# Performance work log

Hardware: AMD Instinct MI355X
Metric: run time of the kernel (lower is better)

Reference implementation:

```python
import jax, jax.numpy as jnp
import numpy as np

DIM = 1024
NUM_HEADS = 16
HEAD_DIM = 64

def setup_inputs() -> dict:
    key = jax.random.key(0)
    ks = jax.random.split(key, 7)
    x = jax.random.normal(ks[0], (4, 4096, DIM), dtype=jnp.float32)
    mask = jnp.ones((4, 4096), dtype=jnp.float32)
    # torch Linear stores weight (out, in) and computes x @ W.T; we store (in, out) directly.
    Wq = jax.random.normal(ks[1], (DIM, NUM_HEADS * HEAD_DIM), dtype=jnp.float32) / np.sqrt(DIM)
    Wk = jax.random.normal(ks[2], (DIM, NUM_HEADS * HEAD_DIM), dtype=jnp.float32) / np.sqrt(DIM)
    Wv = jax.random.normal(ks[3], (DIM, NUM_HEADS * HEAD_DIM), dtype=jnp.float32) / np.sqrt(DIM)
    Wo = jax.random.normal(ks[4], (NUM_HEADS * HEAD_DIM, DIM), dtype=jnp.float32) / np.sqrt(NUM_HEADS * HEAD_DIM)
    # FeatureMap buffer: randn(dim, dim) / sqrt(dim) with dim = head_dim
    proj = jax.random.normal(ks[5], (HEAD_DIM, HEAD_DIM), dtype=jnp.float32) / np.sqrt(HEAD_DIM)
    return {"x": x, "mask": mask, "Wq": Wq, "Wk": Wk, "Wv": Wv, "Wo": Wo, "proj": proj}

def _feature_map(x, proj):
    # phi(x) = elu(x @ proj) + 1  (non-negative random features)
    return jax.nn.elu(x @ proj) + 1.0

def reference(x, mask, Wq, Wk, Wv, Wo, proj):
    b, n, _ = x.shape
    h, d = NUM_HEADS, HEAD_DIM
    # project and split heads: (b, h, n, d)
    q = (x @ Wq).reshape(b, n, h, d).transpose(0, 2, 1, 3)
    k = (x @ Wk).reshape(b, n, h, d).transpose(0, 2, 1, 3)
    v = (x @ Wv).reshape(b, n, h, d).transpose(0, 2, 1, 3)
    q = _feature_map(q, proj)
    k = _feature_map(k, proj)
    # mask: (b, n) -> (b, 1, n, 1)
    k = k * mask[:, None, :, None]
    # linear attention: phi(Q) (phi(K)^T V)
    kv = jnp.einsum('bhnd,bhne->bhde', k, v)          # (b, h, d, d)
    qkv = jnp.einsum('bhnd,bhde->bhne', q, kv)        # (b, h, n, d)
    k_sum = k.sum(axis=2)                              # (b, h, d)
    normalizer = jnp.einsum('bhnd,bhd->bhn', q, k_sum) + 1e-06
    out = qkv / normalizer[..., None]
    out = out.transpose(0, 2, 1, 3).reshape(b, n, h * d)
    return out @ Wo
```

## Files before the change

### kernel.cpp

```cpp
#include <hip/hip_runtime.h>
#include <stdint.h>

#define TOKENS 16384
#define KDIM 1024
#define QKVN 3072

typedef unsigned short u16;
using bf16x8 = __attribute__((ext_vector_type(8))) __bf16;
using f32x4  = __attribute__((ext_vector_type(4))) float;
using u16x8  = __attribute__((ext_vector_type(8))) unsigned short;

__device__ inline u16 f2bf(float f) {
  union { float f; uint32_t u; } v; v.f = f;
  uint32_t u = v.u;
  return (u16)((u + 0x7FFFu + ((u >> 16) & 1u)) >> 16);
}
__device__ inline float bf2f(u16 s) {
  union { uint32_t u; float f; } v; v.u = ((uint32_t)s) << 16;
  return v.f;
}
__device__ inline void g2l16(const void* g, void* l) {
  __builtin_amdgcn_global_load_lds(
      (const __attribute__((address_space(1))) void*)g,
      (__attribute__((address_space(3))) void*)l, 16, 0, 0);
}

template<int LD>
__device__ inline void stage_half(const u16* __restrict__ g, u16* l, int t) {
  #pragma unroll
  for (int i = 0; i < 2; ++i) {
    const int ch = i * 512 + t;
    const int row = ch >> 3;
    const int cc = (ch & 7) ^ (row & 7);
    g2l16(g + (long)row * LD + cc * 8, (char*)l + ch * 16);
  }
}

#define LDA_H(DST, BASE) do { \
  _Pragma("unroll") \
  for (int mi = 0; mi < 4; ++mi) { \
    const int row = wm*64 + mi*16 + rl; \
    const char* p = (const char*)(BASE) + row*128; \
    const int sw = (row & 7) << 4; \
    DST[mi][0] = *(const bf16x8*)(p + ((kg*16) ^ sw)); \
    DST[mi][1] = *(const bf16x8*)(p + ((64 + kg*16) ^ sw)); \
  } \
} while (0)

#define LDB_H(DST, BASE) do { \
  _Pragma("unroll") \
  for (int ni = 0; ni < 2; ++ni) { \
    const int row = wn*32 + ni*16 + rl; \
    const char* p = (const char*)(BASE) + row*128; \
    const int sw = (row & 7) << 4; \
    DST[ni][0] = *(const bf16x8*)(p + ((kg*16) ^ sw)); \
    DST[ni][1] = *(const bf16x8*)(p + ((64 + kg*16) ^ sw)); \
  } \
} while (0)

#define MFMA2Q(MH, AV, BV0, BV1) do { \
  __builtin_amdgcn_s_setprio(1); \
  _Pragma("unroll") \
  for (int kh = 0; kh < 2; ++kh) \
    _Pragma("unroll") \
    for (int mi = 0; mi < 4; ++mi) \
      _Pragma("unroll") \
      for (int ni = 0; ni < 2; ++ni) { \
        acc[(MH)*4+mi][ni]   = __builtin_amdgcn_mfma_f32_16x16x32_bf16( \
            AV[mi][kh], BV0[ni][kh], acc[(MH)*4+mi][ni], 0, 0, 0); \
        acc[(MH)*4+mi][2+ni] = __builtin_amdgcn_mfma_f32_16x16x32_bf16( \
            AV[mi][kh], BV1[ni][kh], acc[(MH)*4+mi][2+ni], 0, 0, 0); \
      } \
  __builtin_amdgcn_s_setprio(0); \
} while (0)

#define LGKM0 do { \
  asm volatile("s_waitcnt lgkmcnt(0)" ::: "memory"); \
  __builtin_amdgcn_sched_barrier(0); \
} while (0)
#define VMC(N) asm volatile("s_waitcnt vmcnt(" #N ")" ::: "memory")
#define BAR() __builtin_amdgcn_s_barrier()

template<int NTOT, int EPI, int ALD, int NT, int PERB>
__device__ __forceinline__ void gemm_body(
    const u16* __restrict__ A, const u16* __restrict__ Bm,
    void* __restrict__ C, const float* __restrict__ aux) {
  __shared__ u16 As[2][2][8192];
  __shared__ u16 Bs[2][2][8192];
  const int t = threadIdx.x;
  const int l = t & 63;
  const int w = t >> 6;
  const int rl = l & 15, kg = l >> 4;
  const int wm = w >> 2, wn = w & 3;
  constexpr int nbn = NTOT / 256;
  constexpr int nwg = 64 * nbn;
  constexpr int GRID = nwg / NT;
  constexpr int KC = NT * 16;
  constexpr int IT = KC / 2;
  static_assert(nwg % 8 == 0, "bijective xcd swizzle");
  const int bid = blockIdx.x;

  auto tcoord = [&](int ot, long& tar, long& tbr) {
    const int gt = ot * GRID + bid;
    const int swz = (gt & 7) * (nwg / 8) + (gt >> 3);
    tar = (long)(swz / nbn) * 256;
    tbr = (long)(swz % nbn) * 256;
  };
  auto asrc = [&](int ch) {
    long ta, tb; tcoord(ch >> 4, ta, tb);
    return A + ta * ALD + (ch & 15) * 64;
  };
  auto bsrc = [&](int ch) {
    long ta, tb; tcoord(ch >> 4, ta, tb);
    return Bm + (PERB ? (ta >> 12) * 1048576 : 0) + tb * 1024 + (ch & 15) * 64;
  };

  f32x4 acc[8][4];
  #pragma unroll
  for (int i = 0; i < 8; ++i)
    #pragma unroll
    for (int j = 0; j < 4; ++j)
      acc[i][j] = (f32x4){0.f, 0.f, 0.f, 0.f};

  bf16x8 afA[4][2], bA[2][2], bB[2][2];

  auto epilogue = [&](int ot) {
    long ar0, br0; tcoord(ot, ar0, br0);
    #pragma unroll
    for (int mh = 0; mh < 2; ++mh)
      #pragma unroll
      for (int mi = 0; mi < 4; ++mi)
        #pragma unroll
        for (int j = 0; j < 4; ++j) {
          const long row = ar0 + mh*128 + wm*64 + mi*16 + kg*4 + j;
          float rs = 0.f;
          if (EPI == 0) rs = aux[row];
          #pragma unroll
          for (int nh = 0; nh < 2; ++nh)
            #pragma unroll
            for (int ni = 0; ni < 2; ++ni) {
              const long col = br0 + nh*128 + wn*32 + ni*16 + rl;
              float v = acc[mh*4+mi][nh*2+ni][j];
              if (EPI == 0) {
                if (col < 2048) {
                  v = (v > 0.f) ? (v + 1.f) : __expf(v);
                  if (col >= 1024) v *= rs;
                }
                ((u16*)C)[row * QKVN + col] = f2bf(v);
              } else {
                ((float*)C)[row * NTOT + col] = v;
              }
            }
        }
    #pragma unroll
    for (int i = 0; i < 8; ++i)
      #pragma unroll
      for (int j = 0; j < 4; ++j)
        acc[i][j] = (f32x4){0.f, 0.f, 0.f, 0.f};
  };

  {
    const u16* A0s = asrc(0); const u16* B0s = bsrc(0);
    const u16* A1s = asrc(1); const u16* B1s = bsrc(1);
    stage_half<ALD >(A0s,             As[0][0], t);
    stage_half<1024>(B0s,             Bs[0][0], t);
    stage_half<1024>(B0s + 128*1024,  Bs[0][1], t);
    stage_half<ALD >(A0s + 128*ALD,   As[0][1], t);
    stage_half<ALD >(A1s,             As[1][0], t);
    stage_half<1024>(B1s,             Bs[1][0], t);
    VMC(4);
    BAR();
  }

  for (int i = 0; i < IT; ++i) {
    const int o1 = 2*i + 1;
    const int e = (2*i + 2 < KC) ? 2*i + 2 : KC - 1;
    const int o = (2*i + 3 < KC) ? 2*i + 3 : KC - 1;
    const u16* Ao1 = asrc(o1); const u16* Bo1 = bsrc(o1);
    const u16* Ae = asrc(e);   const u16* Be = bsrc(e);
    const u16* Ao = asrc(o);   const u16* Bo = bsrc(o);

    LDA_H(afA, As[0][0]); LDB_H(bA, Bs[0][0]); LDB_H(bB, Bs[0][1]);
    stage_half<ALD>(Ao1 + 128*ALD, As[1][1], t);
    stage_half<1024>(Bo1 + 128*1024, Bs[1][1], t);
    LGKM0;
    MFMA2Q(0, afA, bA, bB);
    BAR();

    LDA_H(afA, As[0][1]);
    stage_half<ALD>(Ae, As[0][0], t);
    stage_half<1024>(Be, Bs[0][0], t);
    LGKM0;
    MFMA2Q(1, afA, bA, bB);
    VMC(4); BAR();

    LDA_H(afA, As[1][0]); LDB_H(bA, Bs[1][0]); LDB_H(bB, Bs[1][1]);
    stage_half<ALD>(Ae + 128*ALD, As[0][1], t);
    stage_half<1024>(Be + 128*1024, Bs[0][1], t);
    LGKM0;
    MFMA2Q(0, afA, bA, bB);
    BAR();

    LDA_H(afA, As[1][1]);
    stage_half<ALD>(Ao, As[1][0], t);
    stage_half<1024>(Bo, Bs[1][0], t);
    LGKM0;
    MFMA2Q(1, afA, bA, bB);
    VMC(4); BAR();

    if ((i & 7) == 7) epilogue(i >> 3);
  }
  VMC(0);
}

__global__ __launch_bounds__(512, 2) void gemm_qkv(
    const u16* __restrict__ A, const u16* __restrict__ Bm,
    void* __restrict__ C, const float* __restrict__ aux) {
  gemm_body<3072, 0, 1024, 3, 0>(A, Bm, C, aux);
}
__global__ __launch_bounds__(512, 2) void gemm_out(
    const u16* __restrict__ A, const u16* __restrict__ Bm,
    void* __restrict__ C, const float* __restrict__ aux) {
  gemm_body<1024, 1, 1024, 1, 1>(A, Bm, C, aux);
}

__global__ __launch_bounds__(256) void kv_kernel(const u16* __restrict__ QKV,
    float* __restrict__ kvws, float* __restrict__ ksws) {
  __shared__ u16 Kl[32 * 64];
  __shared__ u16 Vl[32 * 64];
  const int t = threadIdx.x;
  const int l = t & 63, w = t >> 6;
  const int rl = l & 15, kg = l >> 4;
  const int bid = blockIdx.x;
  const int bh = bid >> 4, ns = bid & 15;
  const int b = bh >> 4, h = bh & 15;
  const long tok0 = (long)b * 4096 + ns * 256;

  f32x4 acc[4];
  #pragma unroll
  for (int i = 0; i < 4; ++i) acc[i] = (f32x4){0.f, 0.f, 0.f, 0.f};
  float ks = 0.f;
  const int srow = t >> 3, scc = t & 7;

  for (int it = 0; it < 8; ++it) {
    const long tb = tok0 + it * 32;
    g2l16(QKV + (tb + srow) * QKVN + 1024 + h * 64 + scc * 8, (char*)Kl + t * 16);
    g2l16(QKV + (tb + srow) * QKVN + 2048 + h * 64 + scc * 8, (char*)Vl + t * 16);
    __syncthreads();
    union { u16x8 u; bf16x8 v; } au, bu;
    #pragma unroll
    for (int j = 0; j < 8; ++j) au.u[j] = Kl[(kg * 8 + j) * 64 + w * 16 + rl];
    #pragma unroll
    for (int ni = 0; ni < 4; ++ni) {
      #pragma unroll
      for (int j = 0; j < 8; ++j) bu.u[j] = Vl[(kg * 8 + j) * 64 + ni * 16 + rl];
      acc[ni] = __builtin_amdgcn_mfma_f32_16x16x32_bf16(au.v, bu.v, acc[ni], 0, 0, 0);
    }
    #pragma unroll
    for (int r = 0; r < 8; ++r) ks += bf2f(Kl[(w * 8 + r) * 64 + (t & 63)]);
    __syncthreads();
  }
  float* kvb = kvws + bh * 4096;
  #pragma unroll
  for (int ni = 0; ni < 4; ++ni)
    #pragma unroll
    for (int j = 0; j < 4; ++j) {
      const int d = w * 16 + kg * 4 + j;
      const int e = ni * 16 + rl;
      atomicAdd(&kvb[d * 64 + e], acc[ni][j]);
    }
  atomicAdd(&ksws[bh * 64 + (t & 63)], ks);
}

__global__ __launch_bounds__(256) void finish_kernel(const u16* __restrict__ QKV,
    const float* __restrict__ ksws, const float* __restrict__ kvws,
    const float* __restrict__ Wo, u16* __restrict__ Qc, u16* __restrict__ W2T) {
  __shared__ float sh[4096];
  const int t = threadIdx.x;
  if (blockIdx.x < 1024) {
    const int bid = blockIdx.x;
    const int n0 = bid * 16;
    const int b = n0 >> 12;
    #pragma unroll
    for (int i = 0; i < 4; ++i) sh[i * 256 + t] = ksws[b * 1024 + i * 256 + t];
    __syncthreads();
    const int h = t & 15, ti = t >> 4;
    const u16* qp = QKV + (long)(n0 + ti) * QKVN + h * 64;
    u16* op = Qc + (long)(n0 + ti) * 1024 + h * 64;
    u16x8 v[8];
    float norm = 1e-6f;
    #pragma unroll
    for (int i = 0; i < 8; ++i) {
      v[i] = *(const u16x8*)(qp + i * 8);
      #pragma unroll
      for (int j = 0; j < 8; ++j) norm += bf2f(v[i][j]) * sh[h * 64 + i * 8 + j];
    }
    const float inv = 1.0f / norm;
    #pragma unroll
    for (int i = 0; i < 8; ++i) {
      u16x8 o;
      #pragma unroll
      for (int j = 0; j < 8; ++j) o[j] = f2bf(bf2f(v[i][j]) * inv);
      *(u16x8*)(op + i * 8) = o;
    }
  } else {
    const int bid = blockIdx.x - 1024;
    const int bh = bid >> 2, os = bid & 3;
    const int b = bh >> 4, h = bh & 15;
    const float* kvb = kvws + bh * 4096;
    #pragma unroll
    for (int i = 0; i < 16; ++i) sh[i * 256 + t] = kvb[i * 256 + t];
    __syncthreads();
    const int o = os * 256 + t;
    float wo[64];
    #pragma unroll
    for (int e = 0; e < 64; ++e) wo[e] = Wo[(long)(h * 64 + e) * 1024 + o];
    u16* out = W2T + (long)b * 1048576 + (long)o * 1024 + h * 64;
    for (int d = 0; d < 64; ++d) {
      float s = 0.f;
      #pragma unroll
      for (int e = 0; e < 64; ++e) s += wo[e] * sh[d * 64 + e];
      out[d] = f2bf(s);
    }
  }
}

__global__ __launch_bounds__(256) void prep_w(const float* __restrict__ Wq,
    const float* __restrict__ Wk, const float* __restrict__ proj,
    const float* __restrict__ Wv, const float* __restrict__ x,
    u16* __restrict__ WqkvT, u16* __restrict__ xb) {
  __shared__ float Wl[128][65];
  __shared__ float Pl[64][65];
  const int t = threadIdx.x;
  if (blockIdx.x >= 512) {
    const int idx = (blockIdx.x - 512) * 256 + t;
    const float4* p = (const float4*)x + (long)idx * 2;
    const float4 a = p[0], b = p[1];
    u16x8 o;
    o[0] = f2bf(a.x); o[1] = f2bf(a.y); o[2] = f2bf(a.z); o[3] = f2bf(a.w);
    o[4] = f2bf(b.x); o[5] = f2bf(b.y); o[6] = f2bf(b.z); o[7] = f2bf(b.w);
    *((u16x8*)xb + idx) = o;
    return;
  }
  if (blockIdx.x < 256) {
    const int bid = blockIdx.x;
    const int m = bid >> 7, h = (bid >> 3) & 15, cb = bid & 7;
    const float* W = m ? Wk : Wq;
    #pragma unroll
    for (int i = 0; i < 16; ++i) {
      const int idx = i * 256 + t;
      Pl[idx >> 6][idx & 63] = proj[idx];
    }
    #pragma unroll
    for (int i = 0; i < 32; ++i) {
      const int idx = i * 256 + t;
      const int c = idx >> 6, d = idx & 63;
      Wl[c][d] = W[(long)(cb * 128 + c) * 1024 + h * 64 + d];
    }
    __syncthreads();
    const int c = t & 127, j0 = (t >> 7) * 32;
    float a[32];
    #pragma unroll
    for (int jj = 0; jj < 32; ++jj) a[jj] = 0.f;
    for (int d = 0; d < 64; ++d) {
      const float wv = Wl[c][d];
      #pragma unroll
      for (int jj = 0; jj < 32; ++jj) a[jj] += wv * Pl[d][j0 + jj];
    }
    #pragma unroll
    for (int jj = 0; jj < 32; ++jj)
      WqkvT[(long)(m * 1024 + h * 64 + j0 + jj) * 1024 + cb * 128 + c] = f2bf(a[jj]);
  } else {
    const int bid = blockIdx.x - 256;
    const int rt = (bid >> 4) & 15, ct = bid & 15;
    const int j = t & 63;
    #pragma unroll
    for (int p = 0; p < 16; ++p) {
      const int i = p * 4 + (t >> 6);
      Wl[i][j] = Wv[(long)(rt * 64 + i) * 1024 + ct * 64 + j];
    }
    __syncthreads();
    u16* dst = WqkvT + (long)2048 * 1024;
    #pragma unroll
    for (int p = 0; p < 16; ++p) {
      const int i = p * 4 + (t >> 6);
      dst[(long)(ct * 64 + i) * 1024 + rt * 64 + j] = f2bf(Wl[j][i]);
    }
  }
}

extern "C" void kernel_launch(void* const* d_in, const int* in_sizes, int n_in,
                              void* d_out, int out_size, void* d_ws, size_t ws_size,
                              hipStream_t stream) {
  const float* x    = (const float*)d_in[0];
  const float* mask = (const float*)d_in[1];
  const float* Wq   = (const float*)d_in[2];
  const float* Wk   = (const float*)d_in[3];
  const float* Wv   = (const float*)d_in[4];
  const float* Wo   = (const float*)d_in[5];
  const float* proj = (const float*)d_in[6];

  char* ws = (char*)d_ws;
  u16*  WqkvT = (u16*)(ws);
  u16*  xb    = (u16*)(ws + 8388608);
  u16*  QKV   = (u16*)(ws + 41943040);
  float* kvws = (float*)(ws + 142606336);
  float* ksws = (float*)(ws + 143654912);
  u16*  Qc   = xb;
  u16*  W2T  = (u16*)(ws);
  if (ws_size < (size_t)143671296) return;

  hipMemsetAsync(kvws, 0, 1064960, stream);
  prep_w<<<8704, 256, 0, stream>>>(Wq, Wk, proj, Wv, x, WqkvT, xb);
  gemm_qkv<<<256, 512, 0, stream>>>(xb, WqkvT, (void*)QKV, mask);
  kv_kernel<<<1024, 256, 0, stream>>>(QKV, kvws, ksws);
  finish_kernel<<<1280, 256, 0, stream>>>(QKV, ksws, kvws, Wo, Qc, W2T);
  gemm_out<<<256, 512, 0, stream>>>(Qc, W2T, d_out, nullptr);
}
```

Before: 235.2 us.

## Software-pipeline LDS fragment loads with double register buffers in GEMM mainloop

Adds a second A-fragment register buffer so the next half-tile's LDS reads are issued before the current MFMA block, and waits on partial lgkmcnt instead of draining to zero. B-fragment loads for the next chunk move to after the MFMAs, and global-to-LDS staging of B halves is regrouped with adjusted vmcnt thresholds. The aim is to hide LDS read latency behind MFMA work in both the QKV and output GEMMs. In exchange it raises register pressure under launch_bounds(512,2), and the hand-set wait counts must exactly match the number of outstanding loads or the kernel reads stale data.

```diff
diff --git a/kernel.cpp b/kernel.cpp
--- a/kernel.cpp
+++ b/kernel.cpp
@@ -74,8 +74,8 @@
   __builtin_amdgcn_s_setprio(0); \
 } while (0)
 
-#define LGKM0 do { \
-  asm volatile("s_waitcnt lgkmcnt(0)" ::: "memory"); \
+#define LGKMW(N) do { \
+  asm volatile("s_waitcnt lgkmcnt(" #N ")" ::: "memory"); \
   __builtin_amdgcn_sched_barrier(0); \
 } while (0)
 #define VMC(N) asm volatile("s_waitcnt vmcnt(" #N ")" ::: "memory")
@@ -122,7 +122,7 @@
     for (int j = 0; j < 4; ++j)
       acc[i][j] = (f32x4){0.f, 0.f, 0.f, 0.f};
 
-  bf16x8 afA[4][2], bA[2][2], bB[2][2];
+  bf16x8 afA[4][2], afB[4][2], bA[2][2], bB[2][2];
 
   auto epilogue = [&](int ot) {
     long ar0, br0; tcoord(ot, ar0, br0);
@@ -168,49 +168,62 @@
     stage_half<ALD >(A0s + 128*ALD,   As[0][1], t);
     stage_half<ALD >(A1s,             As[1][0], t);
     stage_half<1024>(B1s,             Bs[1][0], t);
-    VMC(4);
+    stage_half<1024>(B1s + 128*1024,  Bs[1][1], t);
+    VMC(8);
     BAR();
+    LDA_H(afA, As[0][0]);
+    LDB_H(bA, Bs[0][0]);
+    LDB_H(bB, Bs[0][1]);
   }
 
   for (int i = 0; i < IT; ++i) {
     const int o1 = 2*i + 1;
     const int e = (2*i + 2 < KC) ? 2*i + 2 : KC - 1;
     const int o = (2*i + 3 < KC) ? 2*i + 3 : KC - 1;
-    const u16* Ao1 = asrc(o1); const u16* Bo1 = bsrc(o1);
+    const u16* Ao1 = asrc(o1);
     const u16* Ae = asrc(e);   const u16* Be = bsrc(e);
     const u16* Ao = asrc(o);   const u16* Bo = bsrc(o);
 
-    LDA_H(afA, As[0][0]); LDB_H(bA, Bs[0][0]); LDB_H(bB, Bs[0][1]);
+    VMC(6);
+    LDA_H(afB, As[0][1]);
     stage_half<ALD>(Ao1 + 128*ALD, As[1][1], t);
-    stage_half<1024>(Bo1 + 128*1024, Bs[1][1], t);
-    LGKM0;
+    LGKMW(8);
     MFMA2Q(0, afA, bA, bB);
     BAR();
 
-    LDA_H(afA, As[0][1]);
-    stage_half<ALD>(Ae, As[0][0], t);
-    stage_half<1024>(Be, Bs[0][0], t);
-    LGKM0;
-    MFMA2Q(1, afA, bA, bB);
-    VMC(4); BAR();
-
-    LDA_H(afA, As[1][0]); LDB_H(bA, Bs[1][0]); LDB_H(bB, Bs[1][1]);
+    VMC(2);
+    LDA_H(afA, As[1][0]);
+    stage_half<ALD >(Ae,             As[0][0], t);
+    stage_half<1024>(Be,             Bs[0][0], t);
+    stage_half<1024>(Be + 128*1024,  Bs[0][1], t);
+    LGKMW(8);
+    MFMA2Q(1, afB, bA, bB);
+    LDB_H(bA, Bs[1][0]);
+    LDB_H(bB, Bs[1][1]);
+    BAR();
+
+    VMC(6);
+    LDA_H(afB, As[1][1]);
     stage_half<ALD>(Ae + 128*ALD, As[0][1], t);
-    stage_half<1024>(Be + 128*1024, Bs[0][1], t);
-    LGKM0;
+    LGKMW(8);
     MFMA2Q(0, afA, bA, bB);
     BAR();
 
-    LDA_H(afA, As[1][1]);
-    stage_half<ALD>(Ao, As[1][0], t);
-    stage_half<1024>(Bo, Bs[1][0], t);
-    LGKM0;
-    MFMA2Q(1, afA, bA, bB);
-    VMC(4); BAR();
+    VMC(2);
+    LDA_H(afA, As[0][0]);
+    stage_half<ALD >(Ao,             As[1][0], t);
+    stage_half<1024>(Bo,             Bs[1][0], t);
+    stage_half<1024>(Bo + 128*1024,  Bs[1][1], t);
+    LGKMW(8);
+    MFMA2Q(1, afB, bA, bB);
+    LDB_H(bA, Bs[0][0]);
+    LDB_H(bB, Bs[0][1]);
+    BAR();
 
     if ((i & 7) == 7) epilogue(i >> 3);
   }
   VMC(0);
+  LGKMW(0);
 }
 
 __global__ __launch_bounds__(512, 2) void gemm_qkv(
```

New measurement: 259.0 us. +10.1%, slower.
